# Performance work log

Hardware: AMD Instinct MI355X
Metric: run time of the kernel (lower is better)

## Reference

```python
import jax, jax.numpy as jnp
import numpy as np

N = 50000      # nodes
E = 800000     # edges (avg degree 16)
IN = 128
HID = 128
OUT = 64
G = 64         # graphs in batch


def gcn_conv(x, src, dst, W, b, num_nodes):
    # PyG GCNConv: add self-loops, symmetric deg^{-1/2} normalization,
    # linear transform then normalized scatter-add aggregation.
    h = x @ W                                  # [N, H]
    loop = jnp.arange(num_nodes, dtype=src.dtype)
    s = jnp.concatenate([src, loop])           # [E+N]
    d = jnp.concatenate([dst, loop])
    deg = jnp.zeros((num_nodes,), h.dtype).at[d].add(1.0)
    dinv = jax.lax.rsqrt(deg)                  # deg >= 1 thanks to self-loops
    norm = dinv[s] * dinv[d]                   # [E+N]
    msg = h[s] * norm[:, None]                 # gather + scale, [E+N, H]
    out = jnp.zeros_like(h).at[d].add(msg)     # scatter-add
    return out + b


def global_mean_pool(x, batch, num_graphs):
    s = jax.ops.segment_sum(x, batch, num_segments=num_graphs)        # [G, H]
    cnt = jax.ops.segment_sum(jnp.ones((x.shape[0],), x.dtype), batch,
                              num_segments=num_graphs)                 # [G]
    return s / jnp.maximum(cnt, 1.0)[:, None]


def setup_inputs() -> dict:
    key = jax.random.key(0)
    ks = jax.random.split(key, 9)
    x = jax.random.normal(ks[0], (N, IN), jnp.float32)
    ei = jax.random.randint(ks[1], (2, E), 0, N, jnp.int32)
    batch = jnp.sort(jax.random.randint(ks[2], (N,), 0, G, jnp.int32))
    # Glorot-ish init for learned params
    W1 = jax.random.normal(ks[3], (IN, HID), jnp.float32) / np.float32(np.sqrt(IN))
    b1 = jnp.zeros((HID,), jnp.float32)
    W2 = jax.random.normal(ks[4], (HID, HID), jnp.float32) / np.float32(np.sqrt(HID))
    b2 = jnp.zeros((HID,), jnp.float32)
    Wl = jax.random.normal(ks[5], (HID, OUT), jnp.float32) / np.float32(np.sqrt(HID))
    bl = jnp.zeros((OUT,), jnp.float32)
    return {"x": x, "ei": ei, "batch": batch,
            "W1": W1, "b1": b1, "W2": W2, "b2": b2, "Wl": Wl, "bl": bl}


def reference(x, ei, batch, W1, b1, W2, b2, Wl, bl):
    src, dst = ei[0], ei[1]
    h = jax.nn.relu(gcn_conv(x, src, dst, W1, b1, N))
    h = jax.nn.relu(gcn_conv(h, src, dst, W2, b2, N))
    pooled = global_mean_pool(h, batch, G)     # [G, HID]
    return pooled @ Wl + bl                    # [G, OUT]
```

## Files before the change

kernel.cpp:

```cpp
#include <hip/hip_runtime.h>
#include <hip/hip_bf16.h>
#include <cstdint>

#define NN 50000
#define NE 800000
#define HD 128
#define OD 64
#define NG 64
#define NBUCK 196
#define SCHUNK 4096
#define SBLOCKS 196
#define CSR_CAP 5120
#define GEMM_BLOCKS 782

typedef unsigned int uint32;
typedef unsigned short u16;
typedef _Float16 f16;
typedef _Float16 f16x8 __attribute__((ext_vector_type(8)));
typedef float f32x4 __attribute__((ext_vector_type(4)));

static __device__ __forceinline__ u16 f2h(float f) {
    f16 h = (f16)f;
    return __builtin_bit_cast(u16, h);
}
static __device__ __forceinline__ float h2f(u16 u) {
    return (float)__builtin_bit_cast(f16, u);
}
static __device__ __forceinline__ void acc_h2(float2& a, uint32 u) {
    a.x += h2f((u16)(u & 0xffffu));
    a.y += h2f((u16)(u >> 16));
}
static __device__ __forceinline__ uint32 pkh2(float x, float y) {
    return (uint32)f2h(x) | ((uint32)f2h(y) << 16);
}
static __device__ __forceinline__ int swz(int row) {
    return ((row & 7) << 4) | ((row & 8) << 3);
}


__global__ __launch_bounds__(256) void k_prep(const float* __restrict__ W1,
                                              const float* __restrict__ W2,
                                              u16* __restrict__ pw1,
                                              u16* __restrict__ pw2,
                                              int* __restrict__ bucket_fill,
                                              float* __restrict__ pooled) {
    int b = blockIdx.x, t = threadIdx.x;
    if (b == 16) {
        if (t < NBUCK) bucket_fill[t] = 0;
        float4 z = make_float4(0.f, 0.f, 0.f, 0.f);
#pragma unroll
        for (int i = 0; i < 8; ++i) ((float4*)pooled)[i * 256 + t] = z;
        return;
    }
    const float* W = (b < 8) ? W1 : W2;
    u16* pw = (b < 8) ? pw1 : pw2;
    int tau = (b & 7) * 256 + t;
    int lane = tau & 63, ct = (tau >> 6) & 7, ks = (tau >> 9) & 3;
    int g = lane >> 4, n = ct * 16 + (lane & 15);
    uint32 pk[4];
#pragma unroll
    for (int jp = 0; jp < 4; ++jp) {
        int k = ks * 32 + g * 8 + jp * 2;
        uint32 lo = f2h(W[k * 128 + n]);
        uint32 hi = f2h(W[(k + 1) * 128 + n]);
        pk[jp] = lo | (hi << 16);
    }
    ((uint4*)pw)[(size_t)((ks * 8 + ct) * 64 + lane)] = make_uint4(pk[0], pk[1], pk[2], pk[3]);
}


__global__ __launch_bounds__(256) void k_scatter(const int* __restrict__ src,
                                                 const int* __restrict__ dst,
                                                 int* __restrict__ bucket_fill,
                                                 uint32* __restrict__ grec) {
    __shared__ uint32 rin[SCHUNK];
    __shared__ uint32 rout[SCHUNK];
    __shared__ int lh[256], ls[256], lf[256], lgb[256];
    int t = threadIdx.x;
    lh[t] = 0; lf[t] = 0;
    __syncthreads();
    int e0 = blockIdx.x * SCHUNK;
    int ne = min(SCHUNK, NE - e0);
    for (int k = 0; k < 16; ++k) {
        int i = k * 256 + t;
        if (i < ne) {
            uint32 rec = ((uint32)dst[e0 + i] << 16) | (uint32)src[e0 + i];
            rin[i] = rec;
            atomicAdd(&lh[rec >> 24], 1);
        }
    }
    __syncthreads();
    int v = lh[t];
    ls[t] = v; __syncthreads();
    for (int off = 1; off < 256; off <<= 1) {
        int u = (t >= off) ? ls[t - off] : 0;
        __syncthreads();
        ls[t] += u;
        __syncthreads();
    }
    int excl = ls[t] - v;
    __syncthreads();
    ls[t] = excl;
    if (t < NBUCK && v > 0) lgb[t] = atomicAdd(&bucket_fill[t], v);
    __syncthreads();
    for (int k = 0; k < 16; ++k) {
        int i = k * 256 + t;
        if (i < ne) {
            uint32 rec = rin[i];
            int b = rec >> 24;
            int p = ls[b] + atomicAdd(&lf[b], 1);
            rout[p] = rec;
        }
    }
    __syncthreads();
    for (int k = 0; k < 16; ++k) {
        int i = k * 256 + t;
        if (i < ne) {
            uint32 rec = rout[i];
            int b = rec >> 24;
            int pos = lgb[b] + (i - ls[b]);
            if (pos < CSR_CAP) grec[(size_t)b * CSR_CAP + pos] = rec;
        }
    }
}


__global__ __launch_bounds__(256) void k_csr(const uint32* __restrict__ grec,
                                             const int* __restrict__ bucket_fill,
                                             uint32* __restrict__ packed,
                                             float* __restrict__ dinv,
                                             u16* __restrict__ csr) {
    __shared__ uint32 rin[CSR_CAP];
    __shared__ u16 sorted[CSR_CAP];
    __shared__ int cnt_l[256], off_l[256], fill_l[256];
    const int b = blockIdx.x, t = threadIdx.x;
    const int s0 = b * CSR_CAP;
    const int n = min(bucket_fill[b], CSR_CAP);
    cnt_l[t] = 0; fill_l[t] = 0;
    __syncthreads();
    for (int i = t; i < n; i += 256) {
        uint32 r = grec[s0 + i];
        rin[i] = r;
        atomicAdd(&cnt_l[(r >> 16) & 255], 1);
    }
    __syncthreads();
    int v = cnt_l[t];
    off_l[t] = v; __syncthreads();
    for (int off = 1; off < 256; off <<= 1) {
        int u = (t >= off) ? off_l[t - off] : 0;
        __syncthreads();
        off_l[t] += u;
        __syncthreads();
    }
    int excl = off_l[t] - v;
    __syncthreads();
    off_l[t] = excl;
    int vtx = (b << 8) + t;
    if (vtx < NN) {
        packed[vtx] = (uint32)(s0 + excl) | ((uint32)v << 20);
        dinv[vtx] = rsqrtf((float)(v + 1));
    }
    __syncthreads();
    for (int i = t; i < n; i += 256) {
        uint32 r = rin[i];
        int d = (r >> 16) & 255;
        int p = off_l[d] + atomicAdd(&fill_l[d], 1);
        sorted[p] = (u16)(r & 0xffffu);
    }
    __syncthreads();
    for (int i = t; i < n; i += 256) csr[s0 + i] = sorted[i];
}


__global__ __launch_bounds__(256, 2) void k_gemm_f32(const float* __restrict__ X,
                                                     const u16* __restrict__ pw,
                                                     const float* __restrict__ dinv,
                                                     u16* __restrict__ hp, int nrows) {
    __shared__ u16 xp[8192];
    const int t = threadIdx.x, lane = t & 63, wv = t >> 6;
    const int r0 = blockIdx.x * 64;
    const float4* X4 = (const float4*)X;
#pragma unroll
    for (int it = 0; it < 8; ++it) {
        int idx = it * 256 + t;
        int rloc = idx >> 5, kq = idx & 31;
        int rr = r0 + rloc;
        float4 xv = (rr < nrows) ? X4[(size_t)rr * 32 + kq]
                                 : make_float4(0.f, 0.f, 0.f, 0.f);
        int ks = kq >> 3, g = (kq >> 1) & 3, half = kq & 1;
        int wvd = rloc >> 4, ln = (rloc & 15) + 16 * g;
        ushort4 p;
        p.x = f2h(xv.x); p.y = f2h(xv.y); p.z = f2h(xv.z); p.w = f2h(xv.w);
        *(ushort4*)&xp[(((ks * 4 + wvd) * 64 + ln) << 3) + half * 4] = p;
    }
    __syncthreads();
    f32x4 acc[8];
#pragma unroll
    for (int c = 0; c < 8; ++c) acc[c] = (f32x4){0.f, 0.f, 0.f, 0.f};
#pragma unroll
    for (int ks = 0; ks < 4; ++ks) {
        f16x8 a = *reinterpret_cast<f16x8*>(&xp[((ks * 4 + wv) * 64 + lane) << 3]);
#pragma unroll
        for (int ct = 0; ct < 8; ++ct) {
            f16x8 b = *reinterpret_cast<const f16x8*>(pw + ((size_t)((ks * 8 + ct) * 64 + lane) << 3));
            acc[ct] = __builtin_amdgcn_mfma_f32_16x16x32_f16(a, b, acc[ct], 0, 0, 0);
        }
    }
    float dv[4];
#pragma unroll
    for (int r = 0; r < 4; ++r) {
        int m = r0 + wv * 16 + 4 * (lane >> 4) + r;
        dv[r] = (m < nrows) ? dinv[m] : 0.f;
    }
    __syncthreads();
#pragma unroll
    for (int ct = 0; ct < 8; ++ct)
#pragma unroll
        for (int r = 0; r < 4; ++r) {
            int row_local = wv * 16 + 4 * (lane >> 4) + r;
            int colb = ct * 32 + (lane & 15) * 2;
            int byte = row_local * 256 + (colb ^ swz(row_local));
            xp[byte >> 1] = f2h(acc[ct][r] * dv[r]);
        }
    __syncthreads();
#pragma unroll
    for (int p = 0; p < 4; ++p) {
        int row_local = t >> 2;
        int chunk = (t & 3) + 4 * p;
        int byte = row_local * 256 + ((chunk * 16) ^ swz(row_local));
        uint4 val = *reinterpret_cast<uint4*>(&xp[byte >> 1]);
        int rr = r0 + row_local;
        if (rr < nrows) ((uint4*)hp)[(size_t)rr * 16 + chunk] = val;
    }
}


__global__ __launch_bounds__(256, 2) void k_gemm_f16(const u16* __restrict__ Xh,
                                                     const u16* __restrict__ pw,
                                                     const float* __restrict__ dinv,
                                                     u16* __restrict__ hp, int nrows) {
    __shared__ u16 xp[8192];
    const int t = threadIdx.x, lane = t & 63, wv = t >> 6;
    const int r0 = blockIdx.x * 64;
    const uint4* X16 = (const uint4*)Xh;
#pragma unroll
    for (int it = 0; it < 4; ++it) {
        int idx = it * 256 + t;
        int rloc = idx >> 4, c = idx & 15;
        int rr = r0 + rloc;
        uint4 v = (rr < nrows) ? X16[(size_t)rr * 16 + c]
                               : make_uint4(0u, 0u, 0u, 0u);
        int ks = c >> 2, g = c & 3;
        int wvd = rloc >> 4, ln = (rloc & 15) + 16 * g;
        *(uint4*)&xp[((ks * 4 + wvd) * 64 + ln) << 3] = v;
    }
    __syncthreads();
    f32x4 acc[8];
#pragma unroll
    for (int c = 0; c < 8; ++c) acc[c] = (f32x4){0.f, 0.f, 0.f, 0.f};
#pragma unroll
    for (int ks = 0; ks < 4; ++ks) {
        f16x8 a = *reinterpret_cast<f16x8*>(&xp[((ks * 4 + wv) * 64 + lane) << 3]);
#pragma unroll
        for (int ct = 0; ct < 8; ++ct) {
            f16x8 b = *reinterpret_cast<const f16x8*>(pw + ((size_t)((ks * 8 + ct) * 64 + lane) << 3));
            acc[ct] = __builtin_amdgcn_mfma_f32_16x16x32_f16(a, b, acc[ct], 0, 0, 0);
        }
    }
    float dv[4];
#pragma unroll
    for (int r = 0; r < 4; ++r) {
        int m = r0 + wv * 16 + 4 * (lane >> 4) + r;
        dv[r] = (m < nrows) ? dinv[m] : 0.f;
    }
    __syncthreads();
#pragma unroll
    for (int ct = 0; ct < 8; ++ct)
#pragma unroll
        for (int r = 0; r < 4; ++r) {
            int row_local = wv * 16 + 4 * (lane >> 4) + r;
            int colb = ct * 32 + (lane & 15) * 2;
            int byte = row_local * 256 + (colb ^ swz(row_local));
            xp[byte >> 1] = f2h(acc[ct][r] * dv[r]);
        }
    __syncthreads();
#pragma unroll
    for (int p = 0; p < 4; ++p) {
        int row_local = t >> 2;
        int chunk = (t & 3) + 4 * p;
        int byte = row_local * 256 + ((chunk * 16) ^ swz(row_local));
        uint4 val = *reinterpret_cast<uint4*>(&xp[byte >> 1]);
        int rr = r0 + row_local;
        if (rr < nrows) ((uint4*)hp)[(size_t)rr * 16 + chunk] = val;
    }
}


__global__ __launch_bounds__(256) void k_agg(const uint32* __restrict__ hp,
                                             const uint32* __restrict__ packed,
                                             const u16* __restrict__ csr,
                                             const float* __restrict__ dinv,
                                             const float* __restrict__ bias,
                                             uint32* __restrict__ outh) {
    const int lane = threadIdx.x & 63;
    const int v = blockIdx.x * 4 + (threadIdx.x >> 6);
    if (v >= NN) return;
    const int slot = lane >> 4, colg = lane & 15;
    const uint4* hp16 = (const uint4*)hp;

    float acc[8];
#pragma unroll
    for (int j = 0; j < 8; ++j) acc[j] = 0.f;

    if (slot == 0) {
        uint4 m = hp16[(size_t)v * 16 + colg];
        acc[0] += h2f((u16)(m.x & 0xffffu)); acc[1] += h2f((u16)(m.x >> 16));
        acc[2] += h2f((u16)(m.y & 0xffffu)); acc[3] += h2f((u16)(m.y >> 16));
        acc[4] += h2f((u16)(m.z & 0xffffu)); acc[5] += h2f((u16)(m.z >> 16));
        acc[6] += h2f((u16)(m.w & 0xffffu)); acc[7] += h2f((u16)(m.w >> 16));
    }

    uint32 pk = packed[v];
    const int e0 = (int)(pk & 0xFFFFFu);
    const int end = e0 + (int)(pk >> 20);
    int idx = e0 + slot;

    for (; idx + 12 < end; idx += 16) {
        int s0 = csr[idx], s1 = csr[idx + 4], s2 = csr[idx + 8], s3 = csr[idx + 12];
        uint4 m0 = hp16[(size_t)s0 * 16 + colg];
        uint4 m1 = hp16[(size_t)s1 * 16 + colg];
        uint4 m2 = hp16[(size_t)s2 * 16 + colg];
        uint4 m3 = hp16[(size_t)s3 * 16 + colg];
#pragma unroll
        for (int q = 0; q < 4; ++q) {
            uint4 m = (q == 0) ? m0 : (q == 1) ? m1 : (q == 2) ? m2 : m3;
            acc[0] += h2f((u16)(m.x & 0xffffu)); acc[1] += h2f((u16)(m.x >> 16));
            acc[2] += h2f((u16)(m.y & 0xffffu)); acc[3] += h2f((u16)(m.y >> 16));
            acc[4] += h2f((u16)(m.z & 0xffffu)); acc[5] += h2f((u16)(m.z >> 16));
            acc[6] += h2f((u16)(m.w & 0xffffu)); acc[7] += h2f((u16)(m.w >> 16));
        }
    }
    for (; idx < end; idx += 4) {
        int s = csr[idx];
        uint4 m = hp16[(size_t)s * 16 + colg];
        acc[0] += h2f((u16)(m.x & 0xffffu)); acc[1] += h2f((u16)(m.x >> 16));
        acc[2] += h2f((u16)(m.y & 0xffffu)); acc[3] += h2f((u16)(m.y >> 16));
        acc[4] += h2f((u16)(m.z & 0xffffu)); acc[5] += h2f((u16)(m.z >> 16));
        acc[6] += h2f((u16)(m.w & 0xffffu)); acc[7] += h2f((u16)(m.w >> 16));
    }

#pragma unroll
    for (int j = 0; j < 8; ++j) {
        acc[j] += __shfl_xor(acc[j], 16, 64);
        acc[j] += __shfl_xor(acc[j], 32, 64);
    }

    if (slot == 0) {
        float dvv = dinv[v];
        float4 ba = ((const float4*)bias)[colg * 2];
        float4 bb = ((const float4*)bias)[colg * 2 + 1];
        uint4 o;
        o.x = pkh2(fmaxf(acc[0] * dvv + ba.x, 0.f), fmaxf(acc[1] * dvv + ba.y, 0.f));
        o.y = pkh2(fmaxf(acc[2] * dvv + ba.z, 0.f), fmaxf(acc[3] * dvv + ba.w, 0.f));
        o.z = pkh2(fmaxf(acc[4] * dvv + bb.x, 0.f), fmaxf(acc[5] * dvv + bb.y, 0.f));
        o.w = pkh2(fmaxf(acc[6] * dvv + bb.z, 0.f), fmaxf(acc[7] * dvv + bb.w, 0.f));
        ((uint4*)outh)[(size_t)v * 16 + colg] = o;
    }
}


__global__ __launch_bounds__(256) void k_pool1(const uint32* __restrict__ h,
                                               const int* __restrict__ batch,
                                               float* __restrict__ pooled) {
    __shared__ int bl[256];
    const int row0 = blockIdx.x * 256;
    const int rend = min(row0 + 256, NN);
    const int nrows = rend - row0;
    for (int i = threadIdx.x; i < nrows; i += 256) bl[i] = batch[row0 + i];
    __syncthreads();
    const int col2 = threadIdx.x & 63;
    const int rp   = threadIdx.x >> 6;
    float2 acc = make_float2(0.f, 0.f);
    int curg = -1;
    for (int i = rp; i < nrows; i += 4) {
        int g = bl[i];
        if (g != curg) {
            if (curg >= 0) {
                atomicAdd(&pooled[curg * 128 + 2 * col2], acc.x);
                atomicAdd(&pooled[curg * 128 + 2 * col2 + 1], acc.y);
            }
            acc = make_float2(0.f, 0.f);
            curg = g;
        }
        acc_h2(acc, h[(size_t)(row0 + i) * 64 + col2]);
    }
    if (curg >= 0) {
        atomicAdd(&pooled[curg * 128 + 2 * col2], acc.x);
        atomicAdd(&pooled[curg * 128 + 2 * col2 + 1], acc.y);
    }
}


__global__ __launch_bounds__(256) void k_head(const float* __restrict__ pooled,
                                              const int* __restrict__ batch,
                                              const float* __restrict__ Wl,
                                              const float* __restrict__ bl_,
                                              float* __restrict__ out) {
    int g = blockIdx.x, t = threadIdx.x;
    __shared__ int se[2];
    __shared__ float pm[128];
    __shared__ float part[256];
    if (t < 2) {
        int target = g + t;
        int lo = 0, hi = NN;
        while (lo < hi) {
            int mid = (lo + hi) >> 1;
            if (batch[mid] < target) lo = mid + 1; else hi = mid;
        }
        se[t] = lo;
    }
    __syncthreads();
    int cntg = se[1] - se[0];
    float inv = 1.f / (float)(cntg > 0 ? cntg : 1);
    if (t < 128) pm[t] = pooled[g * 128 + t] * inv;
    __syncthreads();
    int col = t & 63, kh = t >> 6;
    float o = 0.f;
    for (int k = kh * 32; k < kh * 32 + 32; ++k) o += pm[k] * Wl[k * OD + col];
    part[t] = o; __syncthreads();
    if (t < OD)
        out[g * OD + t] = part[t] + part[t + 64] + part[t + 128] + part[t + 192] + bl_[t];
}


extern "C" void kernel_launch(void* const* d_in, const int* in_sizes, int n_in,
                              void* d_out, int out_size, void* d_ws, size_t ws_size,
                              hipStream_t stream) {
    const float* x   = (const float*)d_in[0];
    const int*   ei  = (const int*)d_in[1];
    const int*   bat = (const int*)d_in[2];
    const float* W1  = (const float*)d_in[3];
    const float* b1  = (const float*)d_in[4];
    const float* W2  = (const float*)d_in[5];
    const float* b2  = (const float*)d_in[6];
    const float* Wl  = (const float*)d_in[7];
    const float* bl  = (const float*)d_in[8];
    float* out = (float*)d_out;
    const int* src = ei;
    const int* dst = ei + NE;

    char* w = (char*)d_ws;
    size_t off = 0;
    auto alloc = [&](size_t bytes) -> char* {
        char* p = w + off;
        off = (off + bytes + 255) & ~(size_t)255;
        return p;
    };
    float*  dinv        = (float*)alloc(NN * 4);
    uint32* packed      = (uint32*)alloc(NN * 4);
    int*    bucket_fill = (int*)alloc(NBUCK * 4);
    float*  pooled      = (float*)alloc(NG * HD * 4);
    u16*    pw1         = (u16*)alloc(2048 * 16);
    u16*    pw2         = (u16*)alloc(2048 * 16);
    uint32* grec        = (uint32*)alloc((size_t)NBUCK * CSR_CAP * 4);
    u16*    csr         = (u16*)alloc((size_t)NBUCK * CSR_CAP * 2);
    u16*    hp          = (u16*)alloc((size_t)NN * HD * 2);
    u16*    h2          = (u16*)alloc((size_t)NN * HD * 2);

    k_prep<<<17, 256, 0, stream>>>(W1, W2, pw1, pw2, bucket_fill, pooled);
    k_scatter<<<SBLOCKS, 256, 0, stream>>>(src, dst, bucket_fill, grec);
    k_csr<<<NBUCK, 256, 0, stream>>>(grec, bucket_fill, packed, dinv, csr);

    k_gemm_f32<<<GEMM_BLOCKS, 256, 0, stream>>>(x, pw1, dinv, hp, NN);
    k_agg<<<(NN + 3) / 4, 256, 0, stream>>>((const uint32*)hp, packed, csr, dinv, b1, (uint32*)h2);
    k_gemm_f16<<<GEMM_BLOCKS, 256, 0, stream>>>(h2, pw2, dinv, hp, NN);
    k_agg<<<(NN + 3) / 4, 256, 0, stream>>>((const uint32*)hp, packed, csr, dinv, b2, (uint32*)h2);
    k_pool1<<<(NN + 255) / 256, 256, 0, stream>>>((const uint32*)h2, bat, pooled);
    k_head<<<NG, 256, 0, stream>>>(pooled, bat, Wl, bl, out);
}
```

Measured before the change: 152.1 us.

## Fuse layer-1 aggregation into layer-2 GEMM and layer-2 aggregation into pooling

Replaces the separate aggregation, second GEMM and pooling kernels with two fused kernels: one aggregates neighbors for 64 rows directly into shared memory and feeds the MFMA GEMM, the other aggregates layer-2 rows and accumulates the mean-pool sums with atomics. This removes two full intermediate feature-matrix round trips through global memory and two kernel launches. In exchange each wave now processes 16 nodes sequentially with far fewer blocks, reducing the parallelism available to hide gather latency.

```diff
diff --git a/kernel.cpp b/kernel.cpp
--- a/kernel.cpp
+++ b/kernel.cpp
@@ -26,15 +26,51 @@
 static __device__ __forceinline__ float h2f(u16 u) {
     return (float)__builtin_bit_cast(f16, u);
 }
-static __device__ __forceinline__ void acc_h2(float2& a, uint32 u) {
-    a.x += h2f((u16)(u & 0xffffu));
-    a.y += h2f((u16)(u >> 16));
-}
 static __device__ __forceinline__ uint32 pkh2(float x, float y) {
     return (uint32)f2h(x) | ((uint32)f2h(y) << 16);
 }
+static __device__ __forceinline__ void add8(float* a, uint4 m) {
+    a[0] += h2f((u16)(m.x & 0xffffu)); a[1] += h2f((u16)(m.x >> 16));
+    a[2] += h2f((u16)(m.y & 0xffffu)); a[3] += h2f((u16)(m.y >> 16));
+    a[4] += h2f((u16)(m.z & 0xffffu)); a[5] += h2f((u16)(m.z >> 16));
+    a[6] += h2f((u16)(m.w & 0xffffu)); a[7] += h2f((u16)(m.w >> 16));
+}
 static __device__ __forceinline__ int swz(int row) {
     return ((row & 7) << 4) | ((row & 8) << 3);
+}
+
+static __device__ __forceinline__ void agg_node(const uint4* __restrict__ hp16,
+                                                const uint32* __restrict__ packed,
+                                                const u16* __restrict__ csr,
+                                                int v, int slot, int colg, float* acc) {
+#pragma unroll
+    for (int j = 0; j < 8; ++j) acc[j] = 0.f;
+    if (slot == 0) {
+        uint4 m = hp16[(size_t)v * 16 + colg];
+        add8(acc, m);
+    }
+    uint32 pk = packed[v];
+    const int e0 = (int)(pk & 0xFFFFFu);
+    const int end = e0 + (int)(pk >> 20);
+    int idx = e0 + slot;
+    for (; idx + 12 < end; idx += 16) {
+        int s0 = csr[idx], s1 = csr[idx + 4], s2 = csr[idx + 8], s3 = csr[idx + 12];
+        uint4 m0 = hp16[(size_t)s0 * 16 + colg];
+        uint4 m1 = hp16[(size_t)s1 * 16 + colg];
+        uint4 m2 = hp16[(size_t)s2 * 16 + colg];
+        uint4 m3 = hp16[(size_t)s3 * 16 + colg];
+        add8(acc, m0); add8(acc, m1); add8(acc, m2); add8(acc, m3);
+    }
+    for (; idx < end; idx += 4) {
+        int s = csr[idx];
+        uint4 m = hp16[(size_t)s * 16 + colg];
+        add8(acc, m);
+    }
+#pragma unroll
+    for (int j = 0; j < 8; ++j) {
+        acc[j] += __shfl_xor(acc[j], 16, 64);
+        acc[j] += __shfl_xor(acc[j], 32, 64);
+    }
 }
 
 
@@ -235,26 +271,45 @@
 }
 
 
-__global__ __launch_bounds__(256, 2) void k_gemm_f16(const u16* __restrict__ Xh,
-                                                     const u16* __restrict__ pw,
-                                                     const float* __restrict__ dinv,
-                                                     u16* __restrict__ hp, int nrows) {
+__global__ __launch_bounds__(256, 2) void k_aggemm(const uint32* __restrict__ hp,
+                                                   const uint32* __restrict__ packed,
+                                                   const u16* __restrict__ csr,
+                                                   const float* __restrict__ dinv,
+                                                   const float* __restrict__ bias,
+                                                   const u16* __restrict__ pw,
+                                                   u16* __restrict__ hp2, int nrows) {
     __shared__ u16 xp[8192];
     const int t = threadIdx.x, lane = t & 63, wv = t >> 6;
     const int r0 = blockIdx.x * 64;
-    const uint4* X16 = (const uint4*)Xh;
-#pragma unroll
-    for (int it = 0; it < 4; ++it) {
-        int idx = it * 256 + t;
-        int rloc = idx >> 4, c = idx & 15;
-        int rr = r0 + rloc;
-        uint4 v = (rr < nrows) ? X16[(size_t)rr * 16 + c]
-                               : make_uint4(0u, 0u, 0u, 0u);
-        int ks = c >> 2, g = c & 3;
-        int wvd = rloc >> 4, ln = (rloc & 15) + 16 * g;
-        *(uint4*)&xp[((ks * 4 + wvd) * 64 + ln) << 3] = v;
-    }
-    __syncthreads();
+    const int slot = lane >> 4, colg = lane & 15;
+    const uint4* hp16 = (const uint4*)hp;
+    const float4 ba = ((const float4*)bias)[colg * 2];
+    const float4 bb = ((const float4*)bias)[colg * 2 + 1];
+
+    for (int i = 0; i < 16; ++i) {
+        int rloc = wv * 16 + i;
+        int v = r0 + rloc;
+        float acc[8];
+        if (v < NN) {
+            agg_node(hp16, packed, csr, v, slot, colg, acc);
+        } else {
+#pragma unroll
+            for (int j = 0; j < 8; ++j) acc[j] = 0.f;
+        }
+        if (slot == 0) {
+            float dvv = (v < NN) ? dinv[v] : 0.f;
+            uint4 o4;
+            o4.x = pkh2(fmaxf(acc[0] * dvv + ba.x, 0.f), fmaxf(acc[1] * dvv + ba.y, 0.f));
+            o4.y = pkh2(fmaxf(acc[2] * dvv + ba.z, 0.f), fmaxf(acc[3] * dvv + ba.w, 0.f));
+            o4.z = pkh2(fmaxf(acc[4] * dvv + bb.x, 0.f), fmaxf(acc[5] * dvv + bb.y, 0.f));
+            o4.w = pkh2(fmaxf(acc[6] * dvv + bb.z, 0.f), fmaxf(acc[7] * dvv + bb.w, 0.f));
+            if (v >= NN) o4 = make_uint4(0u, 0u, 0u, 0u);
+            int ks = colg >> 2, g = colg & 3, ln = (rloc & 15) + 16 * g;
+            *(uint4*)&xp[((ks * 4 + wv) * 64 + ln) << 3] = o4;
+        }
+    }
+    __syncthreads();
+
     f32x4 acc[8];
 #pragma unroll
     for (int c = 0; c < 8; ++c) acc[c] = (f32x4){0.f, 0.f, 0.f, 0.f};
@@ -291,112 +346,59 @@
         int byte = row_local * 256 + ((chunk * 16) ^ swz(row_local));
         uint4 val = *reinterpret_cast<uint4*>(&xp[byte >> 1]);
         int rr = r0 + row_local;
-        if (rr < nrows) ((uint4*)hp)[(size_t)rr * 16 + chunk] = val;
-    }
-}
-
-
-__global__ __launch_bounds__(256) void k_agg(const uint32* __restrict__ hp,
-                                             const uint32* __restrict__ packed,
-                                             const u16* __restrict__ csr,
-                                             const float* __restrict__ dinv,
-                                             const float* __restrict__ bias,
-                                             uint32* __restrict__ outh) {
-    const int lane = threadIdx.x & 63;
-    const int v = blockIdx.x * 4 + (threadIdx.x >> 6);
-    if (v >= NN) return;
+        if (rr < nrows) ((uint4*)hp2)[(size_t)rr * 16 + chunk] = val;
+    }
+}
+
+
+__global__ __launch_bounds__(256) void k_aggpool(const uint32* __restrict__ hp,
+                                                 const uint32* __restrict__ packed,
+                                                 const u16* __restrict__ csr,
+                                                 const float* __restrict__ dinv,
+                                                 const float* __restrict__ bias,
+                                                 const int* __restrict__ batch,
+                                                 float* __restrict__ pooled) {
+    const int t = threadIdx.x, lane = t & 63, wv = t >> 6;
+    const int r0 = blockIdx.x * 64;
     const int slot = lane >> 4, colg = lane & 15;
     const uint4* hp16 = (const uint4*)hp;
-
-    float acc[8];
-#pragma unroll
-    for (int j = 0; j < 8; ++j) acc[j] = 0.f;
-
-    if (slot == 0) {
-        uint4 m = hp16[(size_t)v * 16 + colg];
-        acc[0] += h2f((u16)(m.x & 0xffffu)); acc[1] += h2f((u16)(m.x >> 16));
-        acc[2] += h2f((u16)(m.y & 0xffffu)); acc[3] += h2f((u16)(m.y >> 16));
-        acc[4] += h2f((u16)(m.z & 0xffffu)); acc[5] += h2f((u16)(m.z >> 16));
-        acc[6] += h2f((u16)(m.w & 0xffffu)); acc[7] += h2f((u16)(m.w >> 16));
-    }
-
-    uint32 pk = packed[v];
-    const int e0 = (int)(pk & 0xFFFFFu);
-    const int end = e0 + (int)(pk >> 20);
-    int idx = e0 + slot;
-
-    for (; idx + 12 < end; idx += 16) {
-        int s0 = csr[idx], s1 = csr[idx + 4], s2 = csr[idx + 8], s3 = csr[idx + 12];
-        uint4 m0 = hp16[(size_t)s0 * 16 + colg];
-        uint4 m1 = hp16[(size_t)s1 * 16 + colg];
-        uint4 m2 = hp16[(size_t)s2 * 16 + colg];
-        uint4 m3 = hp16[(size_t)s3 * 16 + colg];
-#pragma unroll
-        for (int q = 0; q < 4; ++q) {
-            uint4 m = (q == 0) ? m0 : (q == 1) ? m1 : (q == 2) ? m2 : m3;
-            acc[0] += h2f((u16)(m.x & 0xffffu)); acc[1] += h2f((u16)(m.x >> 16));
-            acc[2] += h2f((u16)(m.y & 0xffffu)); acc[3] += h2f((u16)(m.y >> 16));
-            acc[4] += h2f((u16)(m.z & 0xffffu)); acc[5] += h2f((u16)(m.z >> 16));
-            acc[6] += h2f((u16)(m.w & 0xffffu)); acc[7] += h2f((u16)(m.w >> 16));
-        }
-    }
-    for (; idx < end; idx += 4) {
-        int s = csr[idx];
-        uint4 m = hp16[(size_t)s * 16 + colg];
-        acc[0] += h2f((u16)(m.x & 0xffffu)); acc[1] += h2f((u16)(m.x >> 16));
-        acc[2] += h2f((u16)(m.y & 0xffffu)); acc[3] += h2f((u16)(m.y >> 16));
-        acc[4] += h2f((u16)(m.z & 0xffffu)); acc[5] += h2f((u16)(m.z >> 16));
-        acc[6] += h2f((u16)(m.w & 0xffffu)); acc[7] += h2f((u16)(m.w >> 16));
-    }
-
-#pragma unroll
-    for (int j = 0; j < 8; ++j) {
-        acc[j] += __shfl_xor(acc[j], 16, 64);
-        acc[j] += __shfl_xor(acc[j], 32, 64);
-    }
-
-    if (slot == 0) {
+    const float4 ba = ((const float4*)bias)[colg * 2];
+    const float4 bb = ((const float4*)bias)[colg * 2 + 1];
+
+    float pl[8];
+#pragma unroll
+    for (int j = 0; j < 8; ++j) pl[j] = 0.f;
+    int curg = -1;
+
+    for (int i = 0; i < 16; ++i) {
+        int v = r0 + wv * 16 + i;
+        if (v >= NN) break;
+        int g = batch[v];
+        float acc[8];
+        agg_node(hp16, packed, csr, v, slot, colg, acc);
         float dvv = dinv[v];
-        float4 ba = ((const float4*)bias)[colg * 2];
-        float4 bb = ((const float4*)bias)[colg * 2 + 1];
-        uint4 o;
-        o.x = pkh2(fmaxf(acc[0] * dvv + ba.x, 0.f), fmaxf(acc[1] * dvv + ba.y, 0.f));
-        o.y = pkh2(fmaxf(acc[2] * dvv + ba.z, 0.f), fmaxf(acc[3] * dvv + ba.w, 0.f));
-        o.z = pkh2(fmaxf(acc[4] * dvv + bb.x, 0.f), fmaxf(acc[5] * dvv + bb.y, 0.f));
-        o.w = pkh2(fmaxf(acc[6] * dvv + bb.z, 0.f), fmaxf(acc[7] * dvv + bb.w, 0.f));
-        ((uint4*)outh)[(size_t)v * 16 + colg] = o;
-    }
-}
-
-
-__global__ __launch_bounds__(256) void k_pool1(const uint32* __restrict__ h,
-                                               const int* __restrict__ batch,
-                                               float* __restrict__ pooled) {
-    __shared__ int bl[256];
-    const int row0 = blockIdx.x * 256;
-    const int rend = min(row0 + 256, NN);
-    const int nrows = rend - row0;
-    for (int i = threadIdx.x; i < nrows; i += 256) bl[i] = batch[row0 + i];
-    __syncthreads();
-    const int col2 = threadIdx.x & 63;
-    const int rp   = threadIdx.x >> 6;
-    float2 acc = make_float2(0.f, 0.f);
-    int curg = -1;
-    for (int i = rp; i < nrows; i += 4) {
-        int g = bl[i];
+        float o[8];
+        o[0] = fmaxf(acc[0] * dvv + ba.x, 0.f); o[1] = fmaxf(acc[1] * dvv + ba.y, 0.f);
+        o[2] = fmaxf(acc[2] * dvv + ba.z, 0.f); o[3] = fmaxf(acc[3] * dvv + ba.w, 0.f);
+        o[4] = fmaxf(acc[4] * dvv + bb.x, 0.f); o[5] = fmaxf(acc[5] * dvv + bb.y, 0.f);
+        o[6] = fmaxf(acc[6] * dvv + bb.z, 0.f); o[7] = fmaxf(acc[7] * dvv + bb.w, 0.f);
         if (g != curg) {
-            if (curg >= 0) {
-                atomicAdd(&pooled[curg * 128 + 2 * col2], acc.x);
-                atomicAdd(&pooled[curg * 128 + 2 * col2 + 1], acc.y);
+            if (curg >= 0 && slot == 0) {
+#pragma unroll
+                for (int j = 0; j < 8; ++j)
+                    atomicAdd(&pooled[curg * 128 + colg * 8 + j], pl[j]);
             }
-            acc = make_float2(0.f, 0.f);
+#pragma unroll
+            for (int j = 0; j < 8; ++j) pl[j] = 0.f;
             curg = g;
         }
-        acc_h2(acc, h[(size_t)(row0 + i) * 64 + col2]);
-    }
-    if (curg >= 0) {
-        atomicAdd(&pooled[curg * 128 + 2 * col2], acc.x);
-        atomicAdd(&pooled[curg * 128 + 2 * col2 + 1], acc.y);
+#pragma unroll
+        for (int j = 0; j < 8; ++j) pl[j] += o[j];
+    }
+    if (curg >= 0 && slot == 0) {
+#pragma unroll
+        for (int j = 0; j < 8; ++j)
+            atomicAdd(&pooled[curg * 128 + colg * 8 + j], pl[j]);
     }
 }
 
@@ -465,16 +467,14 @@
     uint32* grec        = (uint32*)alloc((size_t)NBUCK * CSR_CAP * 4);
     u16*    csr         = (u16*)alloc((size_t)NBUCK * CSR_CAP * 2);
     u16*    hp          = (u16*)alloc((size_t)NN * HD * 2);
-    u16*    h2          = (u16*)alloc((size_t)NN * HD * 2);
+    u16*    hp2         = (u16*)alloc((size_t)NN * HD * 2);
 
     k_prep<<<17, 256, 0, stream>>>(W1, W2, pw1, pw2, bucket_fill, pooled);
     k_scatter<<<SBLOCKS, 256, 0, stream>>>(src, dst, bucket_fill, grec);
     k_csr<<<NBUCK, 256, 0, stream>>>(grec, bucket_fill, packed, dinv, csr);
 
     k_gemm_f32<<<GEMM_BLOCKS, 256, 0, stream>>>(x, pw1, dinv, hp, NN);
-    k_agg<<<(NN + 3) / 4, 256, 0, stream>>>((const uint32*)hp, packed, csr, dinv, b1, (uint32*)h2);
-    k_gemm_f16<<<GEMM_BLOCKS, 256, 0, stream>>>(h2, pw2, dinv, hp, NN);
-    k_agg<<<(NN + 3) / 4, 256, 0, stream>>>((const uint32*)hp, packed, csr, dinv, b2, (uint32*)h2);
-    k_pool1<<<(NN + 255) / 256, 256, 0, stream>>>((const uint32*)h2, bat, pooled);
+    k_aggemm<<<GEMM_BLOCKS, 256, 0, stream>>>((const uint32*)hp, packed, csr, dinv, b1, pw2, hp2, NN);
+    k_aggpool<<<GEMM_BLOCKS, 256, 0, stream>>>((const uint32*)hp2, packed, csr, dinv, b2, bat, pooled);
     k_head<<<NG, 256, 0, stream>>>(pooled, bat, Wl, bl, out);
 }
```

Result: slower. 173.7 us (+14.2%).

## Split feature matrix into four 32-column slabs and aggregate per slab

Applied to the files above, without the earlier changes.

The node feature buffers move from row-major [N,128] fp16 to four column slabs of 32 features each, stored as [4][N][32]. The GEMM epilogues, GEMM input loads and pooling are updated to match. Aggregation now runs as four block groups, one per slab, with 16 edge slots per wave instead of 4. Each slab is about 3.2 MB, so the random neighbour gathers should hit a smaller working set that fits better in cache. In exchange there are four times as many aggregation blocks, CSR indices and degree info are read once per slab, and the wave reduction needs two extra shuffle stages.

```diff
diff --git a/kernel.cpp b/kernel.cpp
--- a/kernel.cpp
+++ b/kernel.cpp
@@ -12,6 +12,7 @@
 #define SBLOCKS 196
 #define CSR_CAP 5120
 #define GEMM_BLOCKS 782
+#define AGG_NB 12500
 
 typedef unsigned int uint32;
 typedef unsigned short u16;
@@ -26,16 +27,23 @@
 static __device__ __forceinline__ float h2f(u16 u) {
     return (float)__builtin_bit_cast(f16, u);
 }
-static __device__ __forceinline__ void acc_h2(float2& a, uint32 u) {
+static __device__ __forceinline__ uint32 pkh2(float x, float y) {
+    return (uint32)f2h(x) | ((uint32)f2h(y) << 16);
+}
+static __device__ __forceinline__ void acc_h2f2(float2& a, uint32 u) {
     a.x += h2f((u16)(u & 0xffffu));
     a.y += h2f((u16)(u >> 16));
 }
-static __device__ __forceinline__ uint32 pkh2(float x, float y) {
-    return (uint32)f2h(x) | ((uint32)f2h(y) << 16);
+static __device__ __forceinline__ void add8(float* a, uint4 m) {
+    a[0] += h2f((u16)(m.x & 0xffffu)); a[1] += h2f((u16)(m.x >> 16));
+    a[2] += h2f((u16)(m.y & 0xffffu)); a[3] += h2f((u16)(m.y >> 16));
+    a[4] += h2f((u16)(m.z & 0xffffu)); a[5] += h2f((u16)(m.z >> 16));
+    a[6] += h2f((u16)(m.w & 0xffffu)); a[7] += h2f((u16)(m.w >> 16));
 }
 static __device__ __forceinline__ int swz(int row) {
     return ((row & 7) << 4) | ((row & 8) << 3);
 }
+
 
 
 __global__ __launch_bounds__(256) void k_prep(const float* __restrict__ W1,
@@ -230,7 +238,8 @@
         int byte = row_local * 256 + ((chunk * 16) ^ swz(row_local));
         uint4 val = *reinterpret_cast<uint4*>(&xp[byte >> 1]);
         int rr = r0 + row_local;
-        if (rr < nrows) ((uint4*)hp)[(size_t)rr * 16 + chunk] = val;
+        if (rr < nrows)
+            ((uint4*)hp)[((size_t)p * NN + rr) * 4 + (t & 3)] = val;
     }
 }
 
@@ -248,7 +257,7 @@
         int idx = it * 256 + t;
         int rloc = idx >> 4, c = idx & 15;
         int rr = r0 + rloc;
-        uint4 v = (rr < nrows) ? X16[(size_t)rr * 16 + c]
+        uint4 v = (rr < nrows) ? X16[((size_t)(c >> 2) * NN + rr) * 4 + (c & 3)]
                                : make_uint4(0u, 0u, 0u, 0u);
         int ks = c >> 2, g = c & 3;
         int wvd = rloc >> 4, ln = (rloc & 15) + 16 * g;
@@ -291,80 +300,64 @@
         int byte = row_local * 256 + ((chunk * 16) ^ swz(row_local));
         uint4 val = *reinterpret_cast<uint4*>(&xp[byte >> 1]);
         int rr = r0 + row_local;
-        if (rr < nrows) ((uint4*)hp)[(size_t)rr * 16 + chunk] = val;
-    }
-}
-
-
-__global__ __launch_bounds__(256) void k_agg(const uint32* __restrict__ hp,
-                                             const uint32* __restrict__ packed,
-                                             const u16* __restrict__ csr,
-                                             const float* __restrict__ dinv,
-                                             const float* __restrict__ bias,
-                                             uint32* __restrict__ outh) {
+        if (rr < nrows)
+            ((uint4*)hp)[((size_t)p * NN + rr) * 4 + (t & 3)] = val;
+    }
+}
+
+
+__global__ __launch_bounds__(256) void k_aggs(const uint32* __restrict__ hp,
+                                              const uint32* __restrict__ packed,
+                                              const u16* __restrict__ csr,
+                                              const float* __restrict__ dinv,
+                                              const float* __restrict__ bias,
+                                              uint32* __restrict__ outh) {
+    const int p = blockIdx.x / AGG_NB;
+    const int nb = blockIdx.x - p * AGG_NB;
     const int lane = threadIdx.x & 63;
-    const int v = blockIdx.x * 4 + (threadIdx.x >> 6);
-    if (v >= NN) return;
-    const int slot = lane >> 4, colg = lane & 15;
-    const uint4* hp16 = (const uint4*)hp;
+    const int v = nb * 4 + (threadIdx.x >> 6);
+    const int slot = lane >> 2, sub = lane & 3;
+    const uint4* base = (const uint4*)hp + (size_t)p * NN * 4;
 
     float acc[8];
 #pragma unroll
     for (int j = 0; j < 8; ++j) acc[j] = 0.f;
 
     if (slot == 0) {
-        uint4 m = hp16[(size_t)v * 16 + colg];
-        acc[0] += h2f((u16)(m.x & 0xffffu)); acc[1] += h2f((u16)(m.x >> 16));
-        acc[2] += h2f((u16)(m.y & 0xffffu)); acc[3] += h2f((u16)(m.y >> 16));
-        acc[4] += h2f((u16)(m.z & 0xffffu)); acc[5] += h2f((u16)(m.z >> 16));
-        acc[6] += h2f((u16)(m.w & 0xffffu)); acc[7] += h2f((u16)(m.w >> 16));
-    }
-
+        add8(acc, base[(size_t)v * 4 + sub]);
+    }
     uint32 pk = packed[v];
     const int e0 = (int)(pk & 0xFFFFFu);
     const int end = e0 + (int)(pk >> 20);
     int idx = e0 + slot;
-
-    for (; idx + 12 < end; idx += 16) {
-        int s0 = csr[idx], s1 = csr[idx + 4], s2 = csr[idx + 8], s3 = csr[idx + 12];
-        uint4 m0 = hp16[(size_t)s0 * 16 + colg];
-        uint4 m1 = hp16[(size_t)s1 * 16 + colg];
-        uint4 m2 = hp16[(size_t)s2 * 16 + colg];
-        uint4 m3 = hp16[(size_t)s3 * 16 + colg];
-#pragma unroll
-        for (int q = 0; q < 4; ++q) {
-            uint4 m = (q == 0) ? m0 : (q == 1) ? m1 : (q == 2) ? m2 : m3;
-            acc[0] += h2f((u16)(m.x & 0xffffu)); acc[1] += h2f((u16)(m.x >> 16));
-            acc[2] += h2f((u16)(m.y & 0xffffu)); acc[3] += h2f((u16)(m.y >> 16));
-            acc[4] += h2f((u16)(m.z & 0xffffu)); acc[5] += h2f((u16)(m.z >> 16));
-            acc[6] += h2f((u16)(m.w & 0xffffu)); acc[7] += h2f((u16)(m.w >> 16));
-        }
-    }
-    for (; idx < end; idx += 4) {
+    for (; idx + 16 < end; idx += 32) {
+        int s0 = csr[idx], s1 = csr[idx + 16];
+        uint4 m0 = base[(size_t)s0 * 4 + sub];
+        uint4 m1 = base[(size_t)s1 * 4 + sub];
+        add8(acc, m0); add8(acc, m1);
+    }
+    for (; idx < end; idx += 16) {
         int s = csr[idx];
-        uint4 m = hp16[(size_t)s * 16 + colg];
-        acc[0] += h2f((u16)(m.x & 0xffffu)); acc[1] += h2f((u16)(m.x >> 16));
-        acc[2] += h2f((u16)(m.y & 0xffffu)); acc[3] += h2f((u16)(m.y >> 16));
-        acc[4] += h2f((u16)(m.z & 0xffffu)); acc[5] += h2f((u16)(m.z >> 16));
-        acc[6] += h2f((u16)(m.w & 0xffffu)); acc[7] += h2f((u16)(m.w >> 16));
-    }
-
+        add8(acc, base[(size_t)s * 4 + sub]);
+    }
 #pragma unroll
     for (int j = 0; j < 8; ++j) {
+        acc[j] += __shfl_xor(acc[j], 4, 64);
+        acc[j] += __shfl_xor(acc[j], 8, 64);
         acc[j] += __shfl_xor(acc[j], 16, 64);
         acc[j] += __shfl_xor(acc[j], 32, 64);
     }
-
     if (slot == 0) {
         float dvv = dinv[v];
-        float4 ba = ((const float4*)bias)[colg * 2];
-        float4 bb = ((const float4*)bias)[colg * 2 + 1];
+        const float4* b4 = (const float4*)bias;
+        float4 ba = b4[p * 8 + sub * 2];
+        float4 bb = b4[p * 8 + sub * 2 + 1];
         uint4 o;
         o.x = pkh2(fmaxf(acc[0] * dvv + ba.x, 0.f), fmaxf(acc[1] * dvv + ba.y, 0.f));
         o.y = pkh2(fmaxf(acc[2] * dvv + ba.z, 0.f), fmaxf(acc[3] * dvv + ba.w, 0.f));
         o.z = pkh2(fmaxf(acc[4] * dvv + bb.x, 0.f), fmaxf(acc[5] * dvv + bb.y, 0.f));
         o.w = pkh2(fmaxf(acc[6] * dvv + bb.z, 0.f), fmaxf(acc[7] * dvv + bb.w, 0.f));
-        ((uint4*)outh)[(size_t)v * 16 + colg] = o;
+        ((uint4*)outh)[((size_t)p * NN + v) * 4 + sub] = o;
     }
 }
 
@@ -380,6 +373,8 @@
     __syncthreads();
     const int col2 = threadIdx.x & 63;
     const int rp   = threadIdx.x >> 6;
+    const size_t sbase = (size_t)(col2 >> 4) * NN * 16;
+    const int soff = col2 & 15;
     float2 acc = make_float2(0.f, 0.f);
     int curg = -1;
     for (int i = rp; i < nrows; i += 4) {
@@ -392,7 +387,7 @@
             acc = make_float2(0.f, 0.f);
             curg = g;
         }
-        acc_h2(acc, h[(size_t)(row0 + i) * 64 + col2]);
+        acc_h2f2(acc, h[sbase + (size_t)(row0 + i) * 16 + soff]);
     }
     if (curg >= 0) {
         atomicAdd(&pooled[curg * 128 + 2 * col2], acc.x);
@@ -472,9 +467,9 @@
     k_csr<<<NBUCK, 256, 0, stream>>>(grec, bucket_fill, packed, dinv, csr);
 
     k_gemm_f32<<<GEMM_BLOCKS, 256, 0, stream>>>(x, pw1, dinv, hp, NN);
-    k_agg<<<(NN + 3) / 4, 256, 0, stream>>>((const uint32*)hp, packed, csr, dinv, b1, (uint32*)h2);
+    k_aggs<<<4 * AGG_NB, 256, 0, stream>>>((const uint32*)hp, packed, csr, dinv, b1, (uint32*)h2);
     k_gemm_f16<<<GEMM_BLOCKS, 256, 0, stream>>>(h2, pw2, dinv, hp, NN);
-    k_agg<<<(NN + 3) / 4, 256, 0, stream>>>((const uint32*)hp, packed, csr, dinv, b2, (uint32*)h2);
+    k_aggs<<<4 * AGG_NB, 256, 0, stream>>>((const uint32*)hp, packed, csr, dinv, b2, (uint32*)h2);
     k_pool1<<<(NN + 255) / 256, 256, 0, stream>>>((const uint32*)h2, bat, pooled);
     k_head<<<NG, 256, 0, stream>>>(pooled, bat, Wl, bl, out);
 }
```

Result: slower. 243.4 us (+60.1%).
